# Optimization experiments

Hardware: AMD Instinct MI355X
Metric: run time of the kernel (lower is better)

## Reference

```python
import jax, jax.numpy as jnp
import numpy as np

N, E, D, H = 50000, 500000, 128, 128


def setup_inputs() -> dict:
    key = jax.random.key(0)
    ks = jax.random.split(key, 20)
    s = 0.05
    inp = {
        "node_states": jax.random.normal(ks[0], (N, D), jnp.float32),
        "edge_features": jax.random.normal(ks[1], (E, D), jnp.float32),
        "from_idx": jax.random.randint(ks[2], (E,), 0, N, dtype=jnp.int32),
        "to_idx": jax.random.randint(ks[3], (E,), 0, N, dtype=jnp.int32),
        "graph_idx": jax.random.randint(ks[4], (N,), 0, 16, dtype=jnp.int32),
        # message MLP: Linear(3D,H)-ReLU-Linear(H,H)-ReLU-Linear(H,D)
        "mW1": jax.random.normal(ks[5], (3 * D, H), jnp.float32) * s,
        "mb1": jnp.zeros((H,), jnp.float32),
        "mW2": jax.random.normal(ks[6], (H, H), jnp.float32) * s,
        "mb2": jnp.zeros((H,), jnp.float32),
        "mW3": jax.random.normal(ks[7], (H, D), jnp.float32) * s,
        "mb3": jnp.zeros((D,), jnp.float32),
    }
    # three GRU cells; W: input->gates [D,3D], U: hidden->gates [D,3D]; gate order r,z,n (torch)
    for i, g in enumerate(["g0", "g1", "g2"]):
        inp[g + "W"] = jax.random.normal(ks[8 + 2 * i], (D, 3 * D), jnp.float32) * s
        inp[g + "U"] = jax.random.normal(ks[9 + 2 * i], (D, 3 * D), jnp.float32) * s
        inp[g + "b"] = jnp.zeros((3 * D,), jnp.float32)
        inp[g + "c"] = jnp.zeros((3 * D,), jnp.float32)
    return inp


def _mlp(x, W1, b1, W2, b2, W3, b3):
    h = jax.nn.relu(x @ W1 + b1)
    h = jax.nn.relu(h @ W2 + b2)
    return h @ W3 + b3


def _gru(x, h, W, U, b, c):
    gi = x @ W + b  # [N,3D]
    gh = h @ U + c
    ir, iz, inn = jnp.split(gi, 3, axis=1)
    hr, hz, hn = jnp.split(gh, 3, axis=1)
    r = jax.nn.sigmoid(ir + hr)
    z = jax.nn.sigmoid(iz + hz)
    n = jnp.tanh(inn + r * hn)
    return (1.0 - z) * n + z * h


def reference(node_states, edge_features, from_idx, to_idx, graph_idx,
              mW1, mb1, mW2, mb2, mW3, mb3,
              g0W, g0U, g0b, g0c, g1W, g1U, g1b, g1c, g2W, g2U, g2b, g2c):
    n_nodes = node_states.shape[0]

    def prop_once(fi, ti):
        edge_in = jnp.concatenate(
            [node_states[fi], node_states[ti], edge_features], axis=1)  # [E,3D]
        edge_states = _mlp(edge_in, mW1, mb1, mW2, mb2, mW3, mb3)  # [E,D]
        return jax.ops.segment_sum(edge_states, ti, num_segments=n_nodes)

    # forward uses self.message_net for BOTH directions (reverse net unused)
    agg = prop_once(from_idx, to_idx) + prop_once(to_idx, from_idx)  # [N,D]

    h1 = _gru(node_states, agg, g0W, g0U, g0b, g0c)
    h2 = _gru(agg, h1, g1W, g1U, g1b, g1c)
    h3 = _gru(h1, h2, g2W, g2U, g2b, g2c)
    return h3
```

## Files before the change

kernel.cpp:

```cpp
#include <hip/hip_runtime.h>

typedef unsigned short u16;
typedef __attribute__((ext_vector_type(8))) short bf16x8;
typedef __attribute__((ext_vector_type(4))) float f32x4;

__device__ inline u16 f2bf(float f) {
  unsigned int u = __float_as_uint(f);
  u += 0x7fffu + ((u >> 16) & 1u);
  return (u16)(u >> 16);
}
__device__ inline float bf2f(u16 v) {
  return __uint_as_float((unsigned)v << 16);
}

__device__ inline uint4 pack8(float4 a, float4 b) {
  uint4 r;
  r.x = (unsigned)f2bf(a.x) | ((unsigned)f2bf(a.y) << 16);
  r.y = (unsigned)f2bf(a.z) | ((unsigned)f2bf(a.w) << 16);
  r.z = (unsigned)f2bf(b.x) | ((unsigned)f2bf(b.y) << 16);
  r.w = (unsigned)f2bf(b.z) | ((unsigned)f2bf(b.w) << 16);
  return r;
}

__device__ inline void atomic_pk_add_bf16(u16* p, unsigned v) {
  asm volatile("global_atomic_pk_add_bf16 %0, %1, off" : : "v"(p), "v"(v)
               : "memory");
}

struct TransDesc {
  const float* src[9];
  u16* dst[9];
  int R[9];
  int C[9];
  int pre[10];
};

__global__ void transpose_all_kernel(TransDesc td) {
  int t = blockIdx.x * 256 + threadIdx.x;
  if (t >= td.pre[9]) return;
  int seg = 0;
  while (t >= td.pre[seg + 1]) ++seg;
  int local = t - td.pre[seg];
  int C = td.C[seg], R = td.R[seg];
  int r = local / C, c = local - r * C;
  td.dst[seg][(size_t)c * R + r] = f2bf(td.src[seg][local]);
}

__global__ void bf16_to_f32_kernel(const u16* __restrict__ in,
                                   float* __restrict__ out, int n8) {
  int t = blockIdx.x * 256 + threadIdx.x;
  if (t < n8) {
    uint4 v = ((const uint4*)in)[t];
    u16* p = (u16*)&v;
    float4 o0 = {bf2f(p[0]), bf2f(p[1]), bf2f(p[2]), bf2f(p[3])};
    float4 o1 = {bf2f(p[4]), bf2f(p[5]), bf2f(p[6]), bf2f(p[7])};
    ((float4*)out)[t * 2] = o0;
    ((float4*)out)[t * 2 + 1] = o1;
  }
}

__global__ void count_kernel(const int* __restrict__ fi,
                             const int* __restrict__ ti,
                             int* __restrict__ cnt, int E) {
  int e = blockIdx.x * 256 + threadIdx.x;
  if (e < E) {
    atomicAdd(&cnt[ti[e]], 1);
    atomicAdd(&cnt[fi[e]], 1);
  }
}

__global__ void scan1_kernel(const int* __restrict__ cnt,
                             int* __restrict__ partial, int N, int chunk) {
  __shared__ int sdata[256];
  int b = blockIdx.x, t = threadIdx.x;
  int base = b * chunk;
  int sum = 0;
  for (int i = t; i < chunk; i += 256) {
    int idx = base + i;
    if (idx < N) sum += cnt[idx];
  }
  sdata[t] = sum;
  __syncthreads();
  for (int s2 = 128; s2 > 0; s2 >>= 1) {
    if (t < s2) sdata[t] += sdata[t + s2];
    __syncthreads();
  }
  if (t == 0) partial[b] = sdata[0];
}

__global__ void scan2_kernel(int* __restrict__ partial, int* __restrict__ off,
                             int N) {
  __shared__ int s[256];
  int t = threadIdx.x;
  int own = partial[t];
  s[t] = own;
  __syncthreads();
  for (int d2 = 1; d2 < 256; d2 <<= 1) {
    int v = (t >= d2) ? s[t - d2] : 0;
    __syncthreads();
    s[t] += v;
    __syncthreads();
  }
  partial[t] = s[t] - own;
  if (t == 255) off[N] = s[255];
}

__global__ void scan3_kernel(const int* __restrict__ cnt,
                             const int* __restrict__ partialEx,
                             int* __restrict__ off, int* __restrict__ cursor,
                             int N, int chunk) {
  __shared__ int s[256];
  int b = blockIdx.x, t = threadIdx.x;
  int base = b * chunk;
  int own = (t < chunk && base + t < N) ? cnt[base + t] : 0;
  s[t] = own;
  __syncthreads();
  for (int d2 = 1; d2 < 256; d2 <<= 1) {
    int v = (t >= d2) ? s[t - d2] : 0;
    __syncthreads();
    s[t] += v;
    __syncthreads();
  }
  int ex = s[t] - own + partialEx[b];
  if (t < chunk && base + t < N) {
    off[base + t] = ex;
    cursor[base + t] = ex;
  }
}

__global__ void pos_kernel(const int* __restrict__ fi,
                           const int* __restrict__ ti, int* __restrict__ cursor,
                           int* __restrict__ pos0, int* __restrict__ pos1,
                           int E) {
  int e = blockIdx.x * 256 + threadIdx.x;
  if (e < E) {
    pos0[e] = atomicAdd(&cursor[ti[e]], 1);
    pos1[e] = atomicAdd(&cursor[fi[e]], 1);
  }
}

__global__ __launch_bounds__(256) void agg_csr_kernel(
    const u16* __restrict__ msg, const int* __restrict__ off,
    float* __restrict__ aggf, int N) {
  int n = blockIdx.x * 4 + (threadIdx.x >> 6);
  if (n >= N) return;
  int lane = threadIdx.x & 63;
  int s = off[n], e = off[n + 1];
  float a0 = 0.f, a1 = 0.f, b0 = 0.f, b1 = 0.f;
  const unsigned* m32 = (const unsigned*)msg;
  int r = s;
  for (; r + 1 < e; r += 2) {
    unsigned d0 = m32[(size_t)r * 64 + lane];
    unsigned d1 = m32[(size_t)(r + 1) * 64 + lane];
    a0 += bf2f((u16)(d0 & 0xffff));
    a1 += bf2f((u16)(d0 >> 16));
    b0 += bf2f((u16)(d1 & 0xffff));
    b1 += bf2f((u16)(d1 >> 16));
  }
  if (r < e) {
    unsigned d0 = m32[(size_t)r * 64 + lane];
    a0 += bf2f((u16)(d0 & 0xffff));
    a1 += bf2f((u16)(d0 >> 16));
  }
  aggf[(size_t)n * 128 + lane * 2] = a0 + b0;
  aggf[(size_t)n * 128 + lane * 2 + 1] = a1 + b1;
}

__device__ inline void stage_w_rw(u16* sW, const u16* __restrict__ src,
                                  int roww, int colofs, int tid) {
  int n = tid >> 1, half = tid & 1;
  const u16* s = src + (size_t)n * roww + colofs + half * 64;
#pragma unroll
  for (int q = 0; q < 8; ++q) {
    uint4 v = *(const uint4*)(s + q * 8);
    int byte = n * 256 + ((half * 128 + q * 16) ^ ((n & 7) << 4));
    *(uint4*)((char*)sW + byte) = v;
  }
}

__device__ inline void mfma_pass(const u16* A, const u16* W, f32x4 acc[8],
                                 int w, int lane) {
  const int cA = lane & 15;
  const int ko = (lane >> 4) * 8;
  const int arow = 16 * w + cA;
#pragma unroll
  for (int kk = 0; kk < 4; ++kk) {
    int ka = (kk * 32 + ko) * 2;
    int sx = ka ^ ((cA & 7) << 4);
    bf16x8 a = *(const bf16x8*)((const char*)A + arow * 256 + sx);
#pragma unroll
    for (int nt = 0; nt < 8; ++nt) {
      bf16x8 bb = *(const bf16x8*)((const char*)W + (nt * 16 + cA) * 256 + sx);
      acc[nt] = __builtin_amdgcn_mfma_f32_16x16x32_bf16(a, bb, acc[nt], 0, 0, 0);
    }
  }
}

__device__ inline void write_h_lds(u16* sH, const f32x4 acc[8], int w,
                                   int lane) {
#pragma unroll
  for (int nt = 0; nt < 8; ++nt) {
    int col = nt * 16 + (lane & 15);
#pragma unroll
    for (int i = 0; i < 4; ++i) {
      int rr = 16 * w + ((lane >> 4) * 4) + i;
      *(u16*)((char*)sH + rr * 256 + ((col * 2) ^ ((rr & 7) << 4))) =
          f2bf(acc[nt][i]);
    }
  }
}

__device__ inline void stage_w_512(u16* sW, const u16* __restrict__ src,
                                   int roww, int colofs, int tid) {
  int n = tid >> 2, quarter = tid & 3;
  const u16* s = src + (size_t)n * roww + colofs + quarter * 32;
#pragma unroll
  for (int q = 0; q < 4; ++q) {
    uint4 v = *(const uint4*)(s + q * 8);
    int byte = n * 256 + ((quarter * 64 + q * 16) ^ ((n & 7) << 4));
    *(uint4*)((char*)sW + byte) = v;
  }
}

__global__ __launch_bounds__(256) void node_partial_kernel(
    const float* __restrict__ ns, const u16* __restrict__ Wt1,
    u16* __restrict__ Pa, u16* __restrict__ Pb, int N) {
  __shared__ u16 sA[64 * 128];
  __shared__ u16 sW[128 * 128];
  const int tid = threadIdx.x;
  const int lane = tid & 63;
  const int w = tid >> 6;
  const int r0 = blockIdx.x * 64;
  {
    int row = tid >> 2, seg = tid & 3;
    int rr = r0 + row;
    if (rr >= N) rr = N - 1;
    const float4* sx = (const float4*)(ns + (size_t)rr * 128 + seg * 32);
#pragma unroll
    for (int q = 0; q < 4; ++q) {
      int byte = row * 256 + ((seg * 64 + q * 16) ^ ((row & 7) << 4));
      *(uint4*)((char*)sA + byte) = pack8(sx[q * 2], sx[q * 2 + 1]);
    }
  }
  stage_w_rw(sW, Wt1, 384, 0, tid);
  __syncthreads();
  f32x4 accA[8] = {};
  mfma_pass(sA, sW, accA, w, lane);
  __syncthreads();
  stage_w_rw(sW, Wt1, 384, 128, tid);
  __syncthreads();
  f32x4 accB[8] = {};
  mfma_pass(sA, sW, accB, w, lane);
#pragma unroll
  for (int nt = 0; nt < 8; ++nt) {
    int col = nt * 16 + (lane & 15);
#pragma unroll
    for (int i = 0; i < 4; ++i) {
      int rr = 16 * w + ((lane >> 4) * 4) + i;
      int row = r0 + rr;
      if (row < N) {
        Pa[(size_t)row * 128 + col] = f2bf(accA[nt][i]);
        Pb[(size_t)row * 128 + col] = f2bf(accB[nt][i]);
      }
    }
  }
}

template <int MODE>
__global__ __launch_bounds__(512, 2) void edge_fused_kernel(
    const float* __restrict__ ef, const int* __restrict__ from_idx,
    const int* __restrict__ to_idx, const u16* __restrict__ Wt1,
    const u16* __restrict__ Wt2, const u16* __restrict__ Wt3,
    const u16* __restrict__ Pa, const u16* __restrict__ Pb,
    const float* __restrict__ b1, const float* __restrict__ b2,
    const float* __restrict__ b3, const int* __restrict__ pos0,
    const int* __restrict__ pos1, u16* __restrict__ out_buf, int E,
    int ntiles) {
  __shared__ u16 sW1c[128 * 128];
  __shared__ u16 sH[128 * 128];
  __shared__ int sPos[128];
  const int tid = threadIdx.x;
  const int lane = tid & 63;
  const int wv = tid >> 6;
  const int mw = wv >> 1;
  const int nw = wv & 1;
  const int dir = mw >> 1;
  const int l15 = lane & 15;
  const int lhi = lane >> 4;

  stage_w_512(sW1c, Wt1, 384, 256, tid);

  float b1f[4], b2f[4], b3f[4];
#pragma unroll
  for (int nt = 0; nt < 4; ++nt) {
    int col = (nw << 6) + (nt << 4) + l15;
    b1f[nt] = b1[col];
    b2f[nt] = b2[col];
    b3f[nt] = b3[col];
  }
  bf16x8 w2f[4][4], w3f[4][4];
#pragma unroll
  for (int nt = 0; nt < 4; ++nt) {
    int c = (nw << 6) + (nt << 4) + l15;
#pragma unroll
    for (int kk = 0; kk < 4; ++kk) {
      w2f[nt][kk] = *(const bf16x8*)(Wt2 + (size_t)c * 128 + (kk << 5) + (lhi << 3));
      w3f[nt][kk] = *(const bf16x8*)(Wt3 + (size_t)c * 128 + (kk << 5) + (lhi << 3));
    }
  }
  __syncthreads();

  for (int t = blockIdx.x; t < ntiles; t += gridDim.x) {
    const int e0 = t << 6;
    if (MODE == 0 && tid < 128) {
      int er = tid & 63;
      int e = e0 + er;
      int p = -1;
      if (e < E) p = (tid < 64) ? pos0[e] : pos1[e];
      sPos[tid] = p;
    }
    {
      const int arow = (mw << 4) + l15;
      int e = e0 + arow;
      if (e >= E) e = E - 1;
      const float* ep = ef + (size_t)e * 128 + (lhi << 3);
      bf16x8 efA[4];
#pragma unroll
      for (int kk = 0; kk < 4; ++kk) {
        float4 f0 = *(const float4*)(ep + (kk << 5));
        float4 f1 = *(const float4*)(ep + (kk << 5) + 4);
        uint4 u = pack8(f0, f1);
        efA[kk] = *(bf16x8*)&u;
      }
      f32x4 a1[4] = {};
#pragma unroll
      for (int kk = 0; kk < 4; ++kk) {
#pragma unroll
        for (int nt = 0; nt < 4; ++nt) {
          int c = (nw << 6) + (nt << 4) + l15;
          int sx = ((kk << 6) + (lhi << 4)) ^ ((c & 7) << 4);
          bf16x8 bb = *(const bf16x8*)((const char*)sW1c + c * 256 + sx);
          a1[nt] = __builtin_amdgcn_mfma_f32_16x16x32_bf16(efA[kk], bb, a1[nt], 0, 0, 0);
        }
      }
#pragma unroll
      for (int nt = 0; nt < 4; ++nt) {
        int col = (nw << 6) + (nt << 4) + l15;
#pragma unroll
        for (int i = 0; i < 4; ++i) {
          int row = (mw << 4) + (lhi << 2) + i;
          u16 val = f2bf(a1[nt][i] + b1f[nt]);
          int sw = (col * 2) ^ ((row & 7) << 4);
          *(u16*)((char*)sH + row * 256 + sw) = val;
          *(u16*)((char*)sH + (row + 64) * 256 + sw) = val;
        }
      }
    }
    __syncthreads();
#pragma unroll
    for (int it = 0; it < 4; ++it) {
      int row = (tid >> 4) + (it << 5);
      int c8 = tid & 15;
      int er = row & 63, d = row >> 6;
      int ec = e0 + er;
      if (ec >= E) ec = E - 1;
      int fi_e = from_idx[ec], ti_e = to_idx[ec];
      int sA = d ? ti_e : fi_e;
      int sB = d ? fi_e : ti_e;
      char* hptr = (char*)sH + row * 256 + ((c8 << 4) ^ ((row & 7) << 4));
      uint4 efv = *(const uint4*)hptr;
      uint4 pav = *(const uint4*)(Pa + (size_t)sA * 128 + (c8 << 3));
      uint4 pbv = *(const uint4*)(Pb + (size_t)sB * 128 + (c8 << 3));
      const u16* pe = (const u16*)&efv;
      const u16* pa = (const u16*)&pav;
      const u16* pb = (const u16*)&pbv;
      unsigned o[4];
#pragma unroll
      for (int j = 0; j < 4; ++j) {
        float v0 = fmaxf(bf2f(pe[2 * j]) + bf2f(pa[2 * j]) + bf2f(pb[2 * j]), 0.f);
        float v1 = fmaxf(bf2f(pe[2 * j + 1]) + bf2f(pa[2 * j + 1]) + bf2f(pb[2 * j + 1]), 0.f);
        o[j] = (unsigned)f2bf(v0) | ((unsigned)f2bf(v1) << 16);
      }
      *(uint4*)hptr = *(uint4*)o;
    }
    __syncthreads();
    bf16x8 hA[2][4];
#pragma unroll
    for (int m = 0; m < 2; ++m) {
      int ra = (mw << 5) + (m << 4) + l15;
#pragma unroll
      for (int kk = 0; kk < 4; ++kk) {
        int sx = ((kk << 6) + (lhi << 4)) ^ ((ra & 7) << 4);
        hA[m][kk] = *(const bf16x8*)((const char*)sH + ra * 256 + sx);
      }
    }
    f32x4 acc2[2][4] = {};
#pragma unroll
    for (int kk = 0; kk < 4; ++kk)
#pragma unroll
      for (int nt = 0; nt < 4; ++nt)
#pragma unroll
        for (int m = 0; m < 2; ++m)
          acc2[m][nt] = __builtin_amdgcn_mfma_f32_16x16x32_bf16(
              hA[m][kk], w2f[nt][kk], acc2[m][nt], 0, 0, 0);
    __syncthreads();
#pragma unroll
    for (int m = 0; m < 2; ++m) {
#pragma unroll
      for (int i = 0; i < 4; ++i) {
        int rl = (mw << 5) + (m << 4) + (lhi << 2) + i;
#pragma unroll
        for (int nt = 0; nt < 4; ++nt) {
          int col = (nw << 6) + (nt << 4) + l15;
          float v = fmaxf(acc2[m][nt][i] + b2f[nt], 0.f);
          *(u16*)((char*)sH + rl * 256 + ((col * 2) ^ ((rl & 7) << 4))) = f2bf(v);
        }
      }
    }
    __syncthreads();
#pragma unroll
    for (int m = 0; m < 2; ++m) {
      int ra = (mw << 5) + (m << 4) + l15;
#pragma unroll
      for (int kk = 0; kk < 4; ++kk) {
        int sx = ((kk << 6) + (lhi << 4)) ^ ((ra & 7) << 4);
        hA[m][kk] = *(const bf16x8*)((const char*)sH + ra * 256 + sx);
      }
    }
    f32x4 acc3[2][4] = {};
#pragma unroll
    for (int kk = 0; kk < 4; ++kk)
#pragma unroll
      for (int nt = 0; nt < 4; ++nt)
#pragma unroll
        for (int m = 0; m < 2; ++m)
          acc3[m][nt] = __builtin_amdgcn_mfma_f32_16x16x32_bf16(
              hA[m][kk], w3f[nt][kk], acc3[m][nt], 0, 0, 0);

    if (MODE == 0) {
      __syncthreads();
#pragma unroll
      for (int m = 0; m < 2; ++m) {
#pragma unroll
        for (int i = 0; i < 4; ++i) {
          int rl = (mw << 5) + (m << 4) + (lhi << 2) + i;
#pragma unroll
          for (int nt = 0; nt < 4; ++nt) {
            int col = (nw << 6) + (nt << 4) + l15;
            *(u16*)((char*)sH + rl * 256 + ((col * 2) ^ ((rl & 7) << 4))) =
                f2bf(acc3[m][nt][i] + b3f[nt]);
          }
        }
      }
      __syncthreads();
#pragma unroll
      for (int it = 0; it < 4; ++it) {
        int task = tid + (it << 9);
        int row = task >> 4, c8 = task & 15;
        int p = sPos[row];
        if (p >= 0) {
          uint4 v = *(const uint4*)((const char*)sH + row * 256 +
                                    ((c8 << 4) ^ ((row & 7) << 4)));
          *(uint4*)(out_buf + (size_t)p * 128 + (c8 << 3)) = v;
        }
      }
      __syncthreads();
    } else {
#pragma unroll
      for (int m = 0; m < 2; ++m) {
#pragma unroll
        for (int i = 0; i < 4; ++i) {
          int er = ((mw & 1) << 5) + (m << 4) + (lhi << 2) + i;
          int e = e0 + er;
#pragma unroll
          for (int nt = 0; nt < 4; ++nt) {
            int col = (nw << 6) + (nt << 4) + l15;
            float v = acc3[m][nt][i] + b3f[nt];
            float vp = __shfl_xor(v, 1);
            if (e < E && !(lane & 1)) {
              int dest = dir ? from_idx[e] : to_idx[e];
              unsigned d2 = (unsigned)f2bf(v) | ((unsigned)f2bf(vp) << 16);
              atomic_pk_add_bf16(out_buf + (size_t)dest * 128 + col, d2);
            }
          }
        }
      }
      __syncthreads();
    }
  }
}

__global__ __launch_bounds__(256, 2) void gru3_kernel(
    const float* __restrict__ ns, const float* __restrict__ aggf,
    const u16* __restrict__ g0W, const u16* __restrict__ g0U,
    const u16* __restrict__ g1W, const u16* __restrict__ g1U,
    const u16* __restrict__ g2W, const u16* __restrict__ g2U,
    const float* __restrict__ b0, const float* __restrict__ c0,
    const float* __restrict__ b1, const float* __restrict__ c1,
    const float* __restrict__ b2, const float* __restrict__ c2,
    float* __restrict__ out, int N) {
  __shared__ u16 sX[64 * 128];
  __shared__ u16 sG[64 * 128];
  __shared__ u16 sW[128 * 128];
  const int tid = threadIdx.x;
  const int lane = tid & 63;
  const int w = tid >> 6;
  const int r0 = blockIdx.x * 64;
  {
    int row = tid >> 2, seg = tid & 3;
    int rr = r0 + row;
    if (rr >= N) rr = N - 1;
    const float4* sx = (const float4*)(ns + (size_t)rr * 128 + seg * 32);
    const float4* sh = (const float4*)(aggf + (size_t)rr * 128 + seg * 32);
#pragma unroll
    for (int q = 0; q < 4; ++q) {
      int byte = row * 256 + ((seg * 64 + q * 16) ^ ((row & 7) << 4));
      *(uint4*)((char*)sX + byte) = pack8(sx[q * 2], sx[q * 2 + 1]);
      *(uint4*)((char*)sG + byte) = pack8(sh[q * 2], sh[q * 2 + 1]);
    }
  }

  float hpf[8][4];

#define GPASS(SRC, ABUF, ACC)                       \
  __syncthreads();                                  \
  stage_w_rw(sW, (SRC), 128, 0, tid);               \
  __syncthreads();                                  \
  mfma_pass((ABUF), sW, (ACC), w, lane);

  {
    f32x4 ar[8] = {}, az[8] = {}, ai[8] = {}, ah[8] = {};
    GPASS(g0W + 0 * 16384, sX, ar)
    GPASS(g0U + 0 * 16384, sG, ar)
    GPASS(g0W + 1 * 16384, sX, az)
    GPASS(g0U + 1 * 16384, sG, az)
    GPASS(g0W + 2 * 16384, sX, ai)
    GPASS(g0U + 2 * 16384, sG, ah)
    f32x4 h1[8];
#pragma unroll
    for (int nt = 0; nt < 8; ++nt) {
      int col = nt * 16 + (lane & 15);
      float brc = b0[col] + c0[col];
      float bzc = b0[128 + col] + c0[128 + col];
      float bi = b0[256 + col];
      float bc2 = c0[256 + col];
#pragma unroll
      for (int i = 0; i < 4; ++i) {
        int rloc = 16 * w + ((lane >> 4) * 4) + i;
        int row = r0 + rloc;
        int rowc = row < N ? row : N - 1;
        float hf = aggf[(size_t)rowc * 128 + col];
        float rg = 1.f / (1.f + __expf(-(ar[nt][i] + brc)));
        float zg = 1.f / (1.f + __expf(-(az[nt][i] + bzc)));
        float pre = ai[nt][i] + bi + rg * (ah[nt][i] + bc2);
        float ng = 2.f / (1.f + __expf(-2.f * pre)) - 1.f;
        float hv = (1.f - zg) * ng + zg * hf;
        h1[nt][i] = hv;
        hpf[nt][i] = hv;
      }
    }
    write_h_lds(sX, h1, w, lane);
  }
  {
    f32x4 ar[8] = {}, az[8] = {}, ai[8] = {}, ah[8] = {};
    GPASS(g1W + 0 * 16384, sG, ar)
    GPASS(g1U + 0 * 16384, sX, ar)
    GPASS(g1W + 1 * 16384, sG, az)
    GPASS(g1U + 1 * 16384, sX, az)
    GPASS(g1W + 2 * 16384, sG, ai)
    GPASS(g1U + 2 * 16384, sX, ah)
    f32x4 h2[8];
#pragma unroll
    for (int nt = 0; nt < 8; ++nt) {
      int col = nt * 16 + (lane & 15);
      float brc = b1[col] + c1[col];
      float bzc = b1[128 + col] + c1[128 + col];
      float bi = b1[256 + col];
      float bc2 = c1[256 + col];
#pragma unroll
      for (int i = 0; i < 4; ++i) {
        float rg = 1.f / (1.f + __expf(-(ar[nt][i] + brc)));
        float zg = 1.f / (1.f + __expf(-(az[nt][i] + bzc)));
        float pre = ai[nt][i] + bi + rg * (ah[nt][i] + bc2);
        float ng = 2.f / (1.f + __expf(-2.f * pre)) - 1.f;
        float hv = (1.f - zg) * ng + zg * hpf[nt][i];
        h2[nt][i] = hv;
        hpf[nt][i] = hv;
      }
    }
    write_h_lds(sG, h2, w, lane);
  }
  {
    f32x4 ar[8] = {}, az[8] = {}, ai[8] = {}, ah[8] = {};
    GPASS(g2W + 0 * 16384, sX, ar)
    GPASS(g2U + 0 * 16384, sG, ar)
    GPASS(g2W + 1 * 16384, sX, az)
    GPASS(g2U + 1 * 16384, sG, az)
    GPASS(g2W + 2 * 16384, sX, ai)
    GPASS(g2U + 2 * 16384, sG, ah)
#pragma unroll
    for (int nt = 0; nt < 8; ++nt) {
      int col = nt * 16 + (lane & 15);
      float brc = b2[col] + c2[col];
      float bzc = b2[128 + col] + c2[128 + col];
      float bi = b2[256 + col];
      float bc2 = c2[256 + col];
#pragma unroll
      for (int i = 0; i < 4; ++i) {
        int rloc = 16 * w + ((lane >> 4) * 4) + i;
        int row = r0 + rloc;
        if (row < N) {
          float rg = 1.f / (1.f + __expf(-(ar[nt][i] + brc)));
          float zg = 1.f / (1.f + __expf(-(az[nt][i] + bzc)));
          float pre = ai[nt][i] + bi + rg * (ah[nt][i] + bc2);
          float ng = 2.f / (1.f + __expf(-2.f * pre)) - 1.f;
          out[(size_t)row * 128 + col] = (1.f - zg) * ng + zg * hpf[nt][i];
        }
      }
    }
  }
#undef GPASS
}

extern "C" void kernel_launch(void* const* d_in, const int* in_sizes, int n_in,
                              void* d_out, int out_size, void* d_ws,
                              size_t ws_size, hipStream_t stream) {
  const float* ns = (const float*)d_in[0];
  const float* ef = (const float*)d_in[1];
  const int* from_idx = (const int*)d_in[2];
  const int* to_idx = (const int*)d_in[3];
  const float* mW1 = (const float*)d_in[5];
  const float* mb1 = (const float*)d_in[6];
  const float* mW2 = (const float*)d_in[7];
  const float* mb2 = (const float*)d_in[8];
  const float* mW3 = (const float*)d_in[9];
  const float* mb3 = (const float*)d_in[10];
  const float* gW[3] = {(const float*)d_in[11], (const float*)d_in[15], (const float*)d_in[19]};
  const float* gU[3] = {(const float*)d_in[12], (const float*)d_in[16], (const float*)d_in[20]};
  const float* gb[3] = {(const float*)d_in[13], (const float*)d_in[17], (const float*)d_in[21]};
  const float* gc[3] = {(const float*)d_in[14], (const float*)d_in[18], (const float*)d_in[22]};

  const int N = in_sizes[0] / 128;
  const int E = in_sizes[1] / 128;

  char* base = (char*)d_ws;
  size_t cur = 0;
  auto alloc = [&](size_t bytes) {
    size_t p = cur;
    cur = (cur + bytes + 255) & ~(size_t)255;
    return (void*)(base + p);
  };
  float* aggf = (float*)alloc((size_t)N * 128 * 4);
  u16* Pa = (u16*)alloc((size_t)N * 128 * 2);
  u16* Pb = (u16*)alloc((size_t)N * 128 * 2);
  u16* Wt1 = (u16*)alloc(384 * 128 * 2);
  u16* Wt2 = (u16*)alloc(128 * 128 * 2);
  u16* Wt3 = (u16*)alloc(128 * 128 * 2);
  u16 *gWt[3], *gUt[3];
  for (int i = 0; i < 3; ++i) {
    gWt[i] = (u16*)alloc(384 * 128 * 2);
    gUt[i] = (u16*)alloc(384 * 128 * 2);
  }
  int* cnt = (int*)alloc((size_t)N * 4);
  int* off = (int*)alloc((size_t)(N + 1) * 4);
  int* cursor = (int*)alloc((size_t)N * 4);
  int* partial = (int*)alloc(256 * 4);
  int* pos0 = (int*)alloc((size_t)E * 4);
  int* pos1 = (int*)alloc((size_t)E * 4);
  u16* aggb = (u16*)alloc((size_t)N * 128 * 2);
  u16* msg = (u16*)alloc((size_t)2 * E * 128 * 2);
  bool csr_ok = (cur <= ws_size);

  {
    TransDesc td;
    const float* srcs[9] = {mW1, mW2, mW3, gW[0], gU[0], gW[1], gU[1], gW[2], gU[2]};
    u16* dsts[9] = {Wt1, Wt2, Wt3, gWt[0], gUt[0], gWt[1], gUt[1], gWt[2], gUt[2]};
    int Rs[9] = {384, 128, 128, 128, 128, 128, 128, 128, 128};
    int Cs[9] = {128, 128, 128, 384, 384, 384, 384, 384, 384};
    int acc = 0;
    for (int i = 0; i < 9; ++i) {
      td.src[i] = srcs[i];
      td.dst[i] = dsts[i];
      td.R[i] = Rs[i];
      td.C[i] = Cs[i];
      td.pre[i] = acc;
      acc += Rs[i] * Cs[i];
    }
    td.pre[9] = acc;
    transpose_all_kernel<<<(acc + 255) / 256, 256, 0, stream>>>(td);
  }

  node_partial_kernel<<<(N + 63) / 64, 256, 0, stream>>>(ns, Wt1, Pa, Pb, N);

  int ntiles = (E + 63) / 64;

  if (csr_ok) {
    hipMemsetAsync(cnt, 0, (size_t)N * 4, stream);
    count_kernel<<<(E + 255) / 256, 256, 0, stream>>>(from_idx, to_idx, cnt, E);
    int chunk = (N + 255) / 256;
    scan1_kernel<<<256, 256, 0, stream>>>(cnt, partial, N, chunk);
    scan2_kernel<<<1, 256, 0, stream>>>(partial, off, N);
    scan3_kernel<<<256, 256, 0, stream>>>(cnt, partial, off, cursor, N, chunk);
    pos_kernel<<<(E + 255) / 256, 256, 0, stream>>>(from_idx, to_idx, cursor,
                                                    pos0, pos1, E);
    int egrid = ntiles < 512 ? ntiles : 512;
    edge_fused_kernel<0><<<egrid, 512, 0, stream>>>(
        ef, from_idx, to_idx, Wt1, Wt2, Wt3, Pa, Pb, mb1, mb2, mb3, pos0, pos1,
        msg, E, ntiles);
    agg_csr_kernel<<<(N + 3) / 4, 256, 0, stream>>>(msg, off, aggf, N);
  } else {
    hipMemsetAsync(aggb, 0, (size_t)N * 128 * 2, stream);
    int egrid = ntiles < 512 ? ntiles : 512;
    edge_fused_kernel<1><<<egrid, 512, 0, stream>>>(
        ef, from_idx, to_idx, Wt1, Wt2, Wt3, Pa, Pb, mb1, mb2, mb3, pos0, pos1,
        aggb, E, ntiles);
    bf16_to_f32_kernel<<<(N * 16 + 255) / 256, 256, 0, stream>>>(aggb, aggf, N * 16);
  }

  int gblocks = (N + 63) / 64;
  gru3_kernel<<<gblocks, 256, 0, stream>>>(
      ns, aggf, gWt[0], gUt[0], gWt[1], gUt[1], gWt[2], gUt[2], gb[0], gc[0],
      gb[1], gc[1], gb[2], gc[2], (float*)d_out, N);
}
```

Before: 625.4 us.

## Precompute edge-feature layer-1 GEMM once and share across both directions

```diff
diff --git a/kernel.cpp b/kernel.cpp
--- a/kernel.cpp
+++ b/kernel.cpp
@@ -146,24 +146,26 @@
   if (n >= N) return;
   int lane = threadIdx.x & 63;
   int s = off[n], e = off[n + 1];
+  const unsigned* m32 = (const unsigned*)msg;
   float a0 = 0.f, a1 = 0.f, b0 = 0.f, b1 = 0.f;
-  const unsigned* m32 = (const unsigned*)msg;
+  float c0 = 0.f, c1 = 0.f, d0 = 0.f, d1 = 0.f;
   int r = s;
-  for (; r + 1 < e; r += 2) {
-    unsigned d0 = m32[(size_t)r * 64 + lane];
-    unsigned d1 = m32[(size_t)(r + 1) * 64 + lane];
-    a0 += bf2f((u16)(d0 & 0xffff));
-    a1 += bf2f((u16)(d0 >> 16));
-    b0 += bf2f((u16)(d1 & 0xffff));
-    b1 += bf2f((u16)(d1 >> 16));
-  }
-  if (r < e) {
-    unsigned d0 = m32[(size_t)r * 64 + lane];
-    a0 += bf2f((u16)(d0 & 0xffff));
-    a1 += bf2f((u16)(d0 >> 16));
-  }
-  aggf[(size_t)n * 128 + lane * 2] = a0 + b0;
-  aggf[(size_t)n * 128 + lane * 2 + 1] = a1 + b1;
+  for (; r + 3 < e; r += 4) {
+    unsigned x0 = m32[(size_t)r * 64 + lane];
+    unsigned x1 = m32[(size_t)(r + 1) * 64 + lane];
+    unsigned x2 = m32[(size_t)(r + 2) * 64 + lane];
+    unsigned x3 = m32[(size_t)(r + 3) * 64 + lane];
+    a0 += bf2f((u16)(x0 & 0xffff)); a1 += bf2f((u16)(x0 >> 16));
+    b0 += bf2f((u16)(x1 & 0xffff)); b1 += bf2f((u16)(x1 >> 16));
+    c0 += bf2f((u16)(x2 & 0xffff)); c1 += bf2f((u16)(x2 >> 16));
+    d0 += bf2f((u16)(x3 & 0xffff)); d1 += bf2f((u16)(x3 >> 16));
+  }
+  for (; r < e; ++r) {
+    unsigned x0 = m32[(size_t)r * 64 + lane];
+    a0 += bf2f((u16)(x0 & 0xffff)); a1 += bf2f((u16)(x0 >> 16));
+  }
+  aggf[(size_t)n * 128 + lane * 2] = (a0 + b0) + (c0 + d0);
+  aggf[(size_t)n * 128 + lane * 2 + 1] = (a1 + b1) + (c1 + d1);
 }
 
 __device__ inline void stage_w_rw(u16* sW, const u16* __restrict__ src,
@@ -263,6 +265,215 @@
         Pb[(size_t)row * 128 + col] = f2bf(accB[nt][i]);
       }
     }
+  }
+}
+
+__global__ __launch_bounds__(256) void efgemm_kernel(
+    const float* __restrict__ ef, const u16* __restrict__ Wt1,
+    const float* __restrict__ b1, u16* __restrict__ EFm, int E) {
+  __shared__ u16 sA[64 * 128];
+  __shared__ u16 sW[128 * 128];
+  const int tid = threadIdx.x;
+  const int lane = tid & 63;
+  const int w = tid >> 6;
+  const int r0 = blockIdx.x * 64;
+  {
+    int row = tid >> 2, seg = tid & 3;
+    int rr = r0 + row;
+    if (rr >= E) rr = E - 1;
+    const float4* sx = (const float4*)(ef + (size_t)rr * 128 + seg * 32);
+#pragma unroll
+    for (int q = 0; q < 4; ++q) {
+      int byte = row * 256 + ((seg * 64 + q * 16) ^ ((row & 7) << 4));
+      *(uint4*)((char*)sA + byte) = pack8(sx[q * 2], sx[q * 2 + 1]);
+    }
+  }
+  stage_w_rw(sW, Wt1, 384, 256, tid);
+  __syncthreads();
+  f32x4 acc[8] = {};
+  mfma_pass(sA, sW, acc, w, lane);
+  __syncthreads();
+#pragma unroll
+  for (int nt = 0; nt < 8; ++nt) {
+    int col = nt * 16 + (lane & 15);
+    float bv = b1[col];
+#pragma unroll
+    for (int i = 0; i < 4; ++i) {
+      int rr = 16 * w + ((lane >> 4) * 4) + i;
+      *(u16*)((char*)sA + rr * 256 + ((col * 2) ^ ((rr & 7) << 4))) =
+          f2bf(acc[nt][i] + bv);
+    }
+  }
+  __syncthreads();
+#pragma unroll
+  for (int it = 0; it < 4; ++it) {
+    int task = tid + (it << 8);
+    int row = task >> 4, c8 = task & 15;
+    int gr = r0 + row;
+    if (gr < E) {
+      uint4 v = *(const uint4*)((const char*)sA + row * 256 +
+                                ((c8 << 4) ^ ((row & 7) << 4)));
+      *(uint4*)(EFm + (size_t)gr * 128 + (c8 << 3)) = v;
+    }
+  }
+}
+
+__global__ __launch_bounds__(512, 2) void edge_mlp2_kernel(
+    const u16* __restrict__ EFm, const int* __restrict__ from_idx,
+    const int* __restrict__ to_idx, const u16* __restrict__ Wt2,
+    const u16* __restrict__ Wt3, const u16* __restrict__ Pa,
+    const u16* __restrict__ Pb, const float* __restrict__ b2,
+    const float* __restrict__ b3, const int* __restrict__ pos0,
+    const int* __restrict__ pos1, u16* __restrict__ msg, int E, int ntiles) {
+  __shared__ u16 sH[256 * 128];
+  __shared__ int sPos[256];
+  const int tid = threadIdx.x;
+  const int lane = tid & 63;
+  const int wv = tid >> 6;
+  const int mw = wv >> 1;
+  const int nw = wv & 1;
+  const int l15 = lane & 15;
+  const int lhi = lane >> 4;
+
+  float b2f[4], b3f[4];
+#pragma unroll
+  for (int nt = 0; nt < 4; ++nt) {
+    int col = (nw << 6) + (nt << 4) + l15;
+    b2f[nt] = b2[col];
+    b3f[nt] = b3[col];
+  }
+  bf16x8 w2f[4][4], w3f[4][4];
+#pragma unroll
+  for (int nt = 0; nt < 4; ++nt) {
+    int c = (nw << 6) + (nt << 4) + l15;
+#pragma unroll
+    for (int kk = 0; kk < 4; ++kk) {
+      w2f[nt][kk] = *(const bf16x8*)(Wt2 + (size_t)c * 128 + (kk << 5) + (lhi << 3));
+      w3f[nt][kk] = *(const bf16x8*)(Wt3 + (size_t)c * 128 + (kk << 5) + (lhi << 3));
+    }
+  }
+
+  for (int t = blockIdx.x; t < ntiles; t += gridDim.x) {
+    const int e0 = t << 7;
+    if (tid < 256) {
+      int er = tid & 127;
+      int e = e0 + er;
+      int p = -1;
+      if (e < E) p = (tid < 128) ? pos0[e] : pos1[e];
+      sPos[tid] = p;
+    }
+#pragma unroll
+    for (int it = 0; it < 8; ++it) {
+      int row = (tid >> 4) + (it << 5);
+      int c8 = tid & 15;
+      int er = row & 127, d = row >> 7;
+      int ec = e0 + er;
+      if (ec >= E) ec = E - 1;
+      int fi_e = from_idx[ec], ti_e = to_idx[ec];
+      int sA = d ? ti_e : fi_e;
+      int sB = d ? fi_e : ti_e;
+      uint4 efv = *(const uint4*)(EFm + (size_t)ec * 128 + (c8 << 3));
+      uint4 pav = *(const uint4*)(Pa + (size_t)sA * 128 + (c8 << 3));
+      uint4 pbv = *(const uint4*)(Pb + (size_t)sB * 128 + (c8 << 3));
+      const u16* pe = (const u16*)&efv;
+      const u16* pa = (const u16*)&pav;
+      const u16* pb = (const u16*)&pbv;
+      unsigned o[4];
+#pragma unroll
+      for (int j = 0; j < 4; ++j) {
+        float v0 = fmaxf(bf2f(pe[2 * j]) + bf2f(pa[2 * j]) + bf2f(pb[2 * j]), 0.f);
+        float v1 = fmaxf(bf2f(pe[2 * j + 1]) + bf2f(pa[2 * j + 1]) + bf2f(pb[2 * j + 1]), 0.f);
+        o[j] = (unsigned)f2bf(v0) | ((unsigned)f2bf(v1) << 16);
+      }
+      *(uint4*)((char*)sH + row * 256 + ((c8 << 4) ^ ((row & 7) << 4))) = *(uint4*)o;
+    }
+    __syncthreads();
+    f32x4 acc[4][4] = {};
+#pragma unroll
+    for (int half = 0; half < 2; ++half) {
+      bf16x8 hA[2][4];
+#pragma unroll
+      for (int m2 = 0; m2 < 2; ++m2) {
+        int ra = (mw << 6) + (((half << 1) + m2) << 4) + l15;
+#pragma unroll
+        for (int kk = 0; kk < 4; ++kk) {
+          int sx = ((kk << 6) + (lhi << 4)) ^ ((ra & 7) << 4);
+          hA[m2][kk] = *(const bf16x8*)((const char*)sH + ra * 256 + sx);
+        }
+      }
+#pragma unroll
+      for (int kk = 0; kk < 4; ++kk)
+#pragma unroll
+        for (int nt = 0; nt < 4; ++nt)
+#pragma unroll
+          for (int m2 = 0; m2 < 2; ++m2)
+            acc[(half << 1) + m2][nt] = __builtin_amdgcn_mfma_f32_16x16x32_bf16(
+                hA[m2][kk], w2f[nt][kk], acc[(half << 1) + m2][nt], 0, 0, 0);
+    }
+    __syncthreads();
+#pragma unroll
+    for (int m = 0; m < 4; ++m) {
+#pragma unroll
+      for (int i = 0; i < 4; ++i) {
+        int rl = (mw << 6) + (m << 4) + (lhi << 2) + i;
+#pragma unroll
+        for (int nt = 0; nt < 4; ++nt) {
+          int col = (nw << 6) + (nt << 4) + l15;
+          float v = fmaxf(acc[m][nt][i] + b2f[nt], 0.f);
+          *(u16*)((char*)sH + rl * 256 + ((col * 2) ^ ((rl & 7) << 4))) = f2bf(v);
+          acc[m][nt][i] = 0.f;
+        }
+      }
+    }
+    __syncthreads();
+#pragma unroll
+    for (int half = 0; half < 2; ++half) {
+      bf16x8 hA[2][4];
+#pragma unroll
+      for (int m2 = 0; m2 < 2; ++m2) {
+        int ra = (mw << 6) + (((half << 1) + m2) << 4) + l15;
+#pragma unroll
+        for (int kk = 0; kk < 4; ++kk) {
+          int sx = ((kk << 6) + (lhi << 4)) ^ ((ra & 7) << 4);
+          hA[m2][kk] = *(const bf16x8*)((const char*)sH + ra * 256 + sx);
+        }
+      }
+#pragma unroll
+      for (int kk = 0; kk < 4; ++kk)
+#pragma unroll
+        for (int nt = 0; nt < 4; ++nt)
+#pragma unroll
+          for (int m2 = 0; m2 < 2; ++m2)
+            acc[(half << 1) + m2][nt] = __builtin_amdgcn_mfma_f32_16x16x32_bf16(
+                hA[m2][kk], w3f[nt][kk], acc[(half << 1) + m2][nt], 0, 0, 0);
+    }
+    __syncthreads();
+#pragma unroll
+    for (int m = 0; m < 4; ++m) {
+#pragma unroll
+      for (int i = 0; i < 4; ++i) {
+        int rl = (mw << 6) + (m << 4) + (lhi << 2) + i;
+#pragma unroll
+        for (int nt = 0; nt < 4; ++nt) {
+          int col = (nw << 6) + (nt << 4) + l15;
+          *(u16*)((char*)sH + rl * 256 + ((col * 2) ^ ((rl & 7) << 4))) =
+              f2bf(acc[m][nt][i] + b3f[nt]);
+        }
+      }
+    }
+    __syncthreads();
+#pragma unroll
+    for (int it = 0; it < 8; ++it) {
+      int task = tid + (it << 9);
+      int row = task >> 4, c8 = task & 15;
+      int p = sPos[row];
+      if (p >= 0) {
+        uint4 v = *(const uint4*)((const char*)sH + row * 256 +
+                                  ((c8 << 4) ^ ((row & 7) << 4)));
+        *(uint4*)(msg + (size_t)p * 128 + (c8 << 3)) = v;
+      }
+    }
+    __syncthreads();
   }
 }
 
@@ -669,7 +880,11 @@
   int* pos1 = (int*)alloc((size_t)E * 4);
   u16* aggb = (u16*)alloc((size_t)N * 128 * 2);
   u16* msg = (u16*)alloc((size_t)2 * E * 128 * 2);
-  bool csr_ok = (cur <= ws_size);
+  size_t cur_msg = cur;
+  u16* EFm = (u16*)alloc((size_t)E * 128 * 2);
+  size_t cur_efm = cur;
+  bool tier0 = (cur_efm <= ws_size);
+  bool tier1 = (cur_msg <= ws_size);
 
   {
     TransDesc td;
@@ -692,9 +907,7 @@
 
   node_partial_kernel<<<(N + 63) / 64, 256, 0, stream>>>(ns, Wt1, Pa, Pb, N);
 
-  int ntiles = (E + 63) / 64;
-
-  if (csr_ok) {
+  if (tier0) {
     hipMemsetAsync(cnt, 0, (size_t)N * 4, stream);
     count_kernel<<<(E + 255) / 256, 256, 0, stream>>>(from_idx, to_idx, cnt, E);
     int chunk = (N + 255) / 256;
@@ -703,6 +916,23 @@
     scan3_kernel<<<256, 256, 0, stream>>>(cnt, partial, off, cursor, N, chunk);
     pos_kernel<<<(E + 255) / 256, 256, 0, stream>>>(from_idx, to_idx, cursor,
                                                     pos0, pos1, E);
+    efgemm_kernel<<<(E + 63) / 64, 256, 0, stream>>>(ef, Wt1, mb1, EFm, E);
+    int ntiles2 = (E + 127) / 128;
+    int egrid = ntiles2 < 512 ? ntiles2 : 512;
+    edge_mlp2_kernel<<<egrid, 512, 0, stream>>>(EFm, from_idx, to_idx, Wt2,
+                                                Wt3, Pa, Pb, mb2, mb3, pos0,
+                                                pos1, msg, E, ntiles2);
+    agg_csr_kernel<<<(N + 3) / 4, 256, 0, stream>>>(msg, off, aggf, N);
+  } else if (tier1) {
+    hipMemsetAsync(cnt, 0, (size_t)N * 4, stream);
+    count_kernel<<<(E + 255) / 256, 256, 0, stream>>>(from_idx, to_idx, cnt, E);
+    int chunk = (N + 255) / 256;
+    scan1_kernel<<<256, 256, 0, stream>>>(cnt, partial, N, chunk);
+    scan2_kernel<<<1, 256, 0, stream>>>(partial, off, N);
+    scan3_kernel<<<256, 256, 0, stream>>>(cnt, partial, off, cursor, N, chunk);
+    pos_kernel<<<(E + 255) / 256, 256, 0, stream>>>(from_idx, to_idx, cursor,
+                                                    pos0, pos1, E);
+    int ntiles = (E + 63) / 64;
     int egrid = ntiles < 512 ? ntiles : 512;
     edge_fused_kernel<0><<<egrid, 512, 0, stream>>>(
         ef, from_idx, to_idx, Wt1, Wt2, Wt3, Pa, Pb, mb1, mb2, mb3, pos0, pos1,
@@ -710,6 +940,7 @@
     agg_csr_kernel<<<(N + 3) / 4, 256, 0, stream>>>(msg, off, aggf, N);
   } else {
     hipMemsetAsync(aggb, 0, (size_t)N * 128 * 2, stream);
+    int ntiles = (E + 63) / 64;
     int egrid = ntiles < 512 ? ntiles : 512;
     edge_fused_kernel<1><<<egrid, 512, 0, stream>>>(
         ef, from_idx, to_idx, Wt1, Wt2, Wt3, Pa, Pb, mb1, mb2, mb3, pos0, pos1,
```

After: 853.6 us. 36.5% more time.

## Add slim 256-thread edge MLP kernel for CSR path with higher occupancy

Applied to the files above, without the earlier changes.

```diff
diff --git a/kernel.cpp b/kernel.cpp
--- a/kernel.cpp
+++ b/kernel.cpp
@@ -146,24 +146,26 @@
   if (n >= N) return;
   int lane = threadIdx.x & 63;
   int s = off[n], e = off[n + 1];
+  const unsigned* m32 = (const unsigned*)msg;
   float a0 = 0.f, a1 = 0.f, b0 = 0.f, b1 = 0.f;
-  const unsigned* m32 = (const unsigned*)msg;
+  float c0 = 0.f, c1 = 0.f, d0 = 0.f, d1 = 0.f;
   int r = s;
-  for (; r + 1 < e; r += 2) {
-    unsigned d0 = m32[(size_t)r * 64 + lane];
-    unsigned d1 = m32[(size_t)(r + 1) * 64 + lane];
-    a0 += bf2f((u16)(d0 & 0xffff));
-    a1 += bf2f((u16)(d0 >> 16));
-    b0 += bf2f((u16)(d1 & 0xffff));
-    b1 += bf2f((u16)(d1 >> 16));
-  }
-  if (r < e) {
-    unsigned d0 = m32[(size_t)r * 64 + lane];
-    a0 += bf2f((u16)(d0 & 0xffff));
-    a1 += bf2f((u16)(d0 >> 16));
-  }
-  aggf[(size_t)n * 128 + lane * 2] = a0 + b0;
-  aggf[(size_t)n * 128 + lane * 2 + 1] = a1 + b1;
+  for (; r + 3 < e; r += 4) {
+    unsigned x0 = m32[(size_t)r * 64 + lane];
+    unsigned x1 = m32[(size_t)(r + 1) * 64 + lane];
+    unsigned x2 = m32[(size_t)(r + 2) * 64 + lane];
+    unsigned x3 = m32[(size_t)(r + 3) * 64 + lane];
+    a0 += bf2f((u16)(x0 & 0xffff)); a1 += bf2f((u16)(x0 >> 16));
+    b0 += bf2f((u16)(x1 & 0xffff)); b1 += bf2f((u16)(x1 >> 16));
+    c0 += bf2f((u16)(x2 & 0xffff)); c1 += bf2f((u16)(x2 >> 16));
+    d0 += bf2f((u16)(x3 & 0xffff)); d1 += bf2f((u16)(x3 >> 16));
+  }
+  for (; r < e; ++r) {
+    unsigned x0 = m32[(size_t)r * 64 + lane];
+    a0 += bf2f((u16)(x0 & 0xffff)); a1 += bf2f((u16)(x0 >> 16));
+  }
+  aggf[(size_t)n * 128 + lane * 2] = (a0 + b0) + (c0 + d0);
+  aggf[(size_t)n * 128 + lane * 2 + 1] = (a1 + b1) + (c1 + d1);
 }
 
 __device__ inline void stage_w_rw(u16* sW, const u16* __restrict__ src,
@@ -207,18 +209,6 @@
       *(u16*)((char*)sH + rr * 256 + ((col * 2) ^ ((rr & 7) << 4))) =
           f2bf(acc[nt][i]);
     }
-  }
-}
-
-__device__ inline void stage_w_512(u16* sW, const u16* __restrict__ src,
-                                   int roww, int colofs, int tid) {
-  int n = tid >> 2, quarter = tid & 3;
-  const u16* s = src + (size_t)n * roww + colofs + quarter * 32;
-#pragma unroll
-  for (int q = 0; q < 4; ++q) {
-    uint4 v = *(const uint4*)(s + q * 8);
-    int byte = n * 256 + ((quarter * 64 + q * 16) ^ ((n & 7) << 4));
-    *(uint4*)((char*)sW + byte) = v;
   }
 }
 
@@ -266,19 +256,175 @@
   }
 }
 
-template <int MODE>
-__global__ __launch_bounds__(512, 2) void edge_fused_kernel(
+__global__ __launch_bounds__(256, 4) void edge_slim_kernel(
     const float* __restrict__ ef, const int* __restrict__ from_idx,
     const int* __restrict__ to_idx, const u16* __restrict__ Wt1,
     const u16* __restrict__ Wt2, const u16* __restrict__ Wt3,
     const u16* __restrict__ Pa, const u16* __restrict__ Pb,
     const float* __restrict__ b1, const float* __restrict__ b2,
     const float* __restrict__ b3, const int* __restrict__ pos0,
-    const int* __restrict__ pos1, u16* __restrict__ out_buf, int E,
-    int ntiles) {
+    const int* __restrict__ pos1, u16* __restrict__ msg, int E, int ntiles) {
+  __shared__ u16 sH[64 * 128];
+  __shared__ int sPos[64];
+  const int tid = threadIdx.x;
+  const int lane = tid & 63;
+  const int wv = tid >> 6;
+  const int l15 = lane & 15;
+  const int lhi = lane >> 4;
+  const int wrow = wv & 1;
+  const int wcol = wv >> 1;
+
+  float b1f[4], b2f[8], b3f[8];
+#pragma unroll
+  for (int nt = 0; nt < 4; ++nt) b1f[nt] = b1[(wcol << 6) + (nt << 4) + l15];
+#pragma unroll
+  for (int nt = 0; nt < 8; ++nt) {
+    b2f[nt] = b2[(nt << 4) + l15];
+    b3f[nt] = b3[(nt << 4) + l15];
+  }
+
+  for (int t = blockIdx.x; t < ntiles; t += gridDim.x) {
+    const int e0 = t << 5;
+    if (tid < 64) {
+      int er = tid & 31;
+      int e = e0 + er;
+      sPos[tid] = (e < E) ? ((tid < 32) ? pos0[e] : pos1[e]) : -1;
+    }
+    {
+      int arow = (wrow << 4) + l15;
+      int e = e0 + arow;
+      if (e >= E) e = E - 1;
+      const float* ep = ef + (size_t)e * 128 + (lhi << 3);
+      f32x4 a1[4] = {};
+#pragma unroll
+      for (int kk = 0; kk < 4; ++kk) {
+        float4 f0 = *(const float4*)(ep + (kk << 5));
+        float4 f1 = *(const float4*)(ep + (kk << 5) + 4);
+        uint4 u = pack8(f0, f1);
+        bf16x8 av = *(bf16x8*)&u;
+#pragma unroll
+        for (int nt = 0; nt < 4; ++nt) {
+          int c = (wcol << 6) + (nt << 4) + l15;
+          bf16x8 bb = *(const bf16x8*)(Wt1 + (size_t)c * 384 + 256 + (kk << 5) + (lhi << 3));
+          a1[nt] = __builtin_amdgcn_mfma_f32_16x16x32_bf16(av, bb, a1[nt], 0, 0, 0);
+        }
+      }
+#pragma unroll
+      for (int nt = 0; nt < 4; ++nt) {
+        int col = (wcol << 6) + (nt << 4) + l15;
+#pragma unroll
+        for (int i = 0; i < 4; ++i) {
+          int row = (wrow << 4) + (lhi << 2) + i;
+          u16 val = f2bf(a1[nt][i] + b1f[nt]);
+          int sw = (col * 2) ^ ((row & 7) << 4);
+          *(u16*)((char*)sH + row * 256 + sw) = val;
+          *(u16*)((char*)sH + (row + 32) * 256 + sw) = val;
+        }
+      }
+    }
+    __syncthreads();
+#pragma unroll
+    for (int it = 0; it < 4; ++it) {
+      int task = tid + (it << 8);
+      int row = task >> 4;
+      int c8 = task & 15;
+      int er = row & 31, d = row >> 5;
+      int ec = e0 + er;
+      if (ec >= E) ec = E - 1;
+      int fi_e = from_idx[ec], ti_e = to_idx[ec];
+      int sA = d ? ti_e : fi_e;
+      int sB = d ? fi_e : ti_e;
+      char* hptr = (char*)sH + row * 256 + ((c8 << 4) ^ ((row & 7) << 4));
+      uint4 efv = *(const uint4*)hptr;
+      uint4 pav = *(const uint4*)(Pa + (size_t)sA * 128 + (c8 << 3));
+      uint4 pbv = *(const uint4*)(Pb + (size_t)sB * 128 + (c8 << 3));
+      const u16* pe = (const u16*)&efv;
+      const u16* pa = (const u16*)&pav;
+      const u16* pb = (const u16*)&pbv;
+      unsigned o[4];
+#pragma unroll
+      for (int j = 0; j < 4; ++j) {
+        float v0 = fmaxf(bf2f(pe[2 * j]) + bf2f(pa[2 * j]) + bf2f(pb[2 * j]), 0.f);
+        float v1 = fmaxf(bf2f(pe[2 * j + 1]) + bf2f(pa[2 * j + 1]) + bf2f(pb[2 * j + 1]), 0.f);
+        o[j] = (unsigned)f2bf(v0) | ((unsigned)f2bf(v1) << 16);
+      }
+      *(uint4*)hptr = *(uint4*)o;
+    }
+    __syncthreads();
+    const int ra = (wv << 4) + l15;
+    bf16x8 hA[4];
+#pragma unroll
+    for (int kk = 0; kk < 4; ++kk) {
+      int sx = ((kk << 6) + (lhi << 4)) ^ ((ra & 7) << 4);
+      hA[kk] = *(const bf16x8*)((const char*)sH + ra * 256 + sx);
+    }
+    f32x4 acc[8] = {};
+#pragma unroll
+    for (int kk = 0; kk < 4; ++kk) {
+#pragma unroll
+      for (int nt = 0; nt < 8; ++nt) {
+        bf16x8 bb = *(const bf16x8*)(Wt2 + (size_t)((nt << 4) + l15) * 128 + (kk << 5) + (lhi << 3));
+        acc[nt] = __builtin_amdgcn_mfma_f32_16x16x32_bf16(hA[kk], bb, acc[nt], 0, 0, 0);
+      }
+    }
+#pragma unroll
+    for (int nt = 0; nt < 8; ++nt) {
+      int col = (nt << 4) + l15;
+#pragma unroll
+      for (int i = 0; i < 4; ++i) {
+        int rl = (wv << 4) + (lhi << 2) + i;
+        float v = fmaxf(acc[nt][i] + b2f[nt], 0.f);
+        *(u16*)((char*)sH + rl * 256 + ((col * 2) ^ ((rl & 7) << 4))) = f2bf(v);
+        acc[nt][i] = 0.f;
+      }
+    }
+#pragma unroll
+    for (int kk = 0; kk < 4; ++kk) {
+      int sx = ((kk << 6) + (lhi << 4)) ^ ((ra & 7) << 4);
+      hA[kk] = *(const bf16x8*)((const char*)sH + ra * 256 + sx);
+    }
+#pragma unroll
+    for (int kk = 0; kk < 4; ++kk) {
+#pragma unroll
+      for (int nt = 0; nt < 8; ++nt) {
+        bf16x8 bb = *(const bf16x8*)(Wt3 + (size_t)((nt << 4) + l15) * 128 + (kk << 5) + (lhi << 3));
+        acc[nt] = __builtin_amdgcn_mfma_f32_16x16x32_bf16(hA[kk], bb, acc[nt], 0, 0, 0);
+      }
+    }
+#pragma unroll
+    for (int nt = 0; nt < 8; ++nt) {
+      int col = (nt << 4) + l15;
+#pragma unroll
+      for (int i = 0; i < 4; ++i) {
+        int rl = (wv << 4) + (lhi << 2) + i;
+        *(u16*)((char*)sH + rl * 256 + ((col * 2) ^ ((rl & 7) << 4))) =
+            f2bf(acc[nt][i] + b3f[nt]);
+      }
+    }
+#pragma unroll
+    for (int it = 0; it < 4; ++it) {
+      int row = (wv << 4) + (lane >> 4) + (it << 2);
+      int c8 = lane & 15;
+      int p = sPos[row];
+      if (p >= 0) {
+        uint4 v = *(const uint4*)((const char*)sH + row * 256 +
+                                  ((c8 << 4) ^ ((row & 7) << 4)));
+        *(uint4*)(msg + (size_t)p * 128 + (c8 << 3)) = v;
+      }
+    }
+    __syncthreads();
+  }
+}
+
+__global__ __launch_bounds__(512, 2) void edge_atomic_kernel(
+    const float* __restrict__ ef, const int* __restrict__ from_idx,
+    const int* __restrict__ to_idx, const u16* __restrict__ Wt1,
+    const u16* __restrict__ Wt2, const u16* __restrict__ Wt3,
+    const u16* __restrict__ Pa, const u16* __restrict__ Pb,
+    const float* __restrict__ b1, const float* __restrict__ b2,
+    const float* __restrict__ b3, u16* __restrict__ aggb, int E, int ntiles) {
   __shared__ u16 sW1c[128 * 128];
   __shared__ u16 sH[128 * 128];
-  __shared__ int sPos[128];
   const int tid = threadIdx.x;
   const int lane = tid & 63;
   const int wv = tid >> 6;
@@ -288,8 +434,16 @@
   const int l15 = lane & 15;
   const int lhi = lane >> 4;
 
-  stage_w_512(sW1c, Wt1, 384, 256, tid);
-
+  {
+    int n = tid >> 2, quarter = tid & 3;
+    const u16* s = Wt1 + (size_t)n * 384 + 256 + quarter * 32;
+#pragma unroll
+    for (int q = 0; q < 4; ++q) {
+      uint4 v = *(const uint4*)(s + q * 8);
+      int byte = n * 256 + ((quarter * 64 + q * 16) ^ ((n & 7) << 4));
+      *(uint4*)((char*)sW1c + byte) = v;
+    }
+  }
   float b1f[4], b2f[4], b3f[4];
 #pragma unroll
   for (int nt = 0; nt < 4; ++nt) {
@@ -312,13 +466,6 @@
 
   for (int t = blockIdx.x; t < ntiles; t += gridDim.x) {
     const int e0 = t << 6;
-    if (MODE == 0 && tid < 128) {
-      int er = tid & 63;
-      int e = e0 + er;
-      int p = -1;
-      if (e < E) p = (tid < 64) ? pos0[e] : pos1[e];
-      sPos[tid] = p;
-    }
     {
       const int arow = (mw << 4) + l15;
       int e = e0 + arow;
@@ -436,57 +583,26 @@
         for (int m = 0; m < 2; ++m)
           acc3[m][nt] = __builtin_amdgcn_mfma_f32_16x16x32_bf16(
               hA[m][kk], w3f[nt][kk], acc3[m][nt], 0, 0, 0);
-
-    if (MODE == 0) {
-      __syncthreads();
-#pragma unroll
-      for (int m = 0; m < 2; ++m) {
-#pragma unroll
-        for (int i = 0; i < 4; ++i) {
-          int rl = (mw << 5) + (m << 4) + (lhi << 2) + i;
-#pragma unroll
-          for (int nt = 0; nt < 4; ++nt) {
-            int col = (nw << 6) + (nt << 4) + l15;
-            *(u16*)((char*)sH + rl * 256 + ((col * 2) ^ ((rl & 7) << 4))) =
-                f2bf(acc3[m][nt][i] + b3f[nt]);
+#pragma unroll
+    for (int m = 0; m < 2; ++m) {
+#pragma unroll
+      for (int i = 0; i < 4; ++i) {
+        int er = ((mw & 1) << 5) + (m << 4) + (lhi << 2) + i;
+        int e = e0 + er;
+#pragma unroll
+        for (int nt = 0; nt < 4; ++nt) {
+          int col = (nw << 6) + (nt << 4) + l15;
+          float v = acc3[m][nt][i] + b3f[nt];
+          float vp = __shfl_xor(v, 1);
+          if (e < E && !(lane & 1)) {
+            int dest = dir ? from_idx[e] : to_idx[e];
+            unsigned d2 = (unsigned)f2bf(v) | ((unsigned)f2bf(vp) << 16);
+            atomic_pk_add_bf16(aggb + (size_t)dest * 128 + col, d2);
           }
         }
       }
-      __syncthreads();
-#pragma unroll
-      for (int it = 0; it < 4; ++it) {
-        int task = tid + (it << 9);
-        int row = task >> 4, c8 = task & 15;
-        int p = sPos[row];
-        if (p >= 0) {
-          uint4 v = *(const uint4*)((const char*)sH + row * 256 +
-                                    ((c8 << 4) ^ ((row & 7) << 4)));
-          *(uint4*)(out_buf + (size_t)p * 128 + (c8 << 3)) = v;
-        }
-      }
-      __syncthreads();
-    } else {
-#pragma unroll
-      for (int m = 0; m < 2; ++m) {
-#pragma unroll
-        for (int i = 0; i < 4; ++i) {
-          int er = ((mw & 1) << 5) + (m << 4) + (lhi << 2) + i;
-          int e = e0 + er;
-#pragma unroll
-          for (int nt = 0; nt < 4; ++nt) {
-            int col = (nw << 6) + (nt << 4) + l15;
-            float v = acc3[m][nt][i] + b3f[nt];
-            float vp = __shfl_xor(v, 1);
-            if (e < E && !(lane & 1)) {
-              int dest = dir ? from_idx[e] : to_idx[e];
-              unsigned d2 = (unsigned)f2bf(v) | ((unsigned)f2bf(vp) << 16);
-              atomic_pk_add_bf16(out_buf + (size_t)dest * 128 + col, d2);
-            }
-          }
-        }
-      }
-      __syncthreads();
-    }
+    }
+    __syncthreads();
   }
 }
 
@@ -692,8 +808,6 @@
 
   node_partial_kernel<<<(N + 63) / 64, 256, 0, stream>>>(ns, Wt1, Pa, Pb, N);
 
-  int ntiles = (E + 63) / 64;
-
   if (csr_ok) {
     hipMemsetAsync(cnt, 0, (size_t)N * 4, stream);
     count_kernel<<<(E + 255) / 256, 256, 0, stream>>>(from_idx, to_idx, cnt, E);
@@ -703,17 +817,19 @@
     scan3_kernel<<<256, 256, 0, stream>>>(cnt, partial, off, cursor, N, chunk);
     pos_kernel<<<(E + 255) / 256, 256, 0, stream>>>(from_idx, to_idx, cursor,
                                                     pos0, pos1, E);
-    int egrid = ntiles < 512 ? ntiles : 512;
-    edge_fused_kernel<0><<<egrid, 512, 0, stream>>>(
+    int ntiles = (E + 31) / 32;
+    int egrid = ntiles < 1280 ? ntiles : 1280;
+    edge_slim_kernel<<<egrid, 256, 0, stream>>>(
         ef, from_idx, to_idx, Wt1, Wt2, Wt3, Pa, Pb, mb1, mb2, mb3, pos0, pos1,
         msg, E, ntiles);
     agg_csr_kernel<<<(N + 3) / 4, 256, 0, stream>>>(msg, off, aggf, N);
   } else {
     hipMemsetAsync(aggb, 0, (size_t)N * 128 * 2, stream);
+    int ntiles = (E + 63) / 64;
     int egrid = ntiles < 512 ? ntiles : 512;
-    edge_fused_kernel<1><<<egrid, 512, 0, stream>>>(
-        ef, from_idx, to_idx, Wt1, Wt2, Wt3, Pa, Pb, mb1, mb2, mb3, pos0, pos1,
-        aggb, E, ntiles);
+    edge_atomic_kernel<<<egrid, 512, 0, stream>>>(
+        ef, from_idx, to_idx, Wt1, Wt2, Wt3, Pa, Pb, mb1, mb2, mb3, aggb, E,
+        ntiles);
     bf16_to_f32_kernel<<<(N * 16 + 255) / 256, 256, 0, stream>>>(aggb, aggf, N * 16);
   }
 
```

New measurement: 1.951 ms. +211.9%, slower.
